# Optimization experiments

Measured on AMD Instinct MI355X. Metric: run time of the kernel, lower is better.

## Reference

```python
import jax, jax.numpy as jnp
import numpy as np

N_NODES = 100000
N_EDGES = 1_600_000
IN_C, HID_C, CLS_C = 128, 256, 64


def setup_inputs() -> dict:
    key = jax.random.key(0)
    ks = jax.random.split(key, 8)
    x = jax.random.normal(ks[0], (N_NODES, IN_C), dtype=jnp.float32)
    edge_index = jax.random.randint(ks[1], (2, N_EDGES), 0, N_NODES, dtype=jnp.int64)
    s1 = 1.0 / np.sqrt(IN_C)
    s2 = 1.0 / np.sqrt(HID_C)
    W1l = jax.random.uniform(ks[2], (IN_C, HID_C), jnp.float32, -s1, s1)
    W1r = jax.random.uniform(ks[3], (IN_C, HID_C), jnp.float32, -s1, s1)
    b1 = jnp.zeros((HID_C,), jnp.float32)
    W2l = jax.random.uniform(ks[4], (HID_C, CLS_C), jnp.float32, -s2, s2)
    W2r = jax.random.uniform(ks[5], (HID_C, CLS_C), jnp.float32, -s2, s2)
    b2 = jnp.zeros((CLS_C,), jnp.float32)
    return {"x": x, "edge_index": edge_index,
            "W1l": W1l, "W1r": W1r, "b1": b1,
            "W2l": W2l, "W2r": W2r, "b2": b2}


def _sage_conv(x, src, dst, Wl, Wr, b, num_nodes):
    # mean aggregation of source features onto destination nodes
    agg = jax.ops.segment_sum(x[src], dst, num_segments=num_nodes)  # [N, F]
    deg = jax.ops.segment_sum(jnp.ones((src.shape[0], 1), x.dtype), dst,
                              num_segments=num_nodes)               # [N, 1]
    agg = agg / jnp.maximum(deg, 1.0)  # zero-degree nodes -> 0
    return agg @ Wl + x @ Wr + b


def reference(x, edge_index, W1l, W1r, b1, W2l, W2r, b2):
    src, dst = edge_index[0], edge_index[1]
    n = x.shape[0]
    h = jax.nn.relu(_sage_conv(x, src, dst, W1l, W1r, b1, n))
    # dropout(p=0.5) is identity in eval mode
    out = _sage_conv(h, src, dst, W2l, W2r, b2, n)
    return jax.nn.sigmoid(out)
```

## Files before the change

### kernel.cpp

```cpp
#include <hip/hip_runtime.h>

typedef __attribute__((ext_vector_type(8))) short short8;
typedef __attribute__((ext_vector_type(4))) float floatx4;
typedef __attribute__((ext_vector_type(2))) float floatx2;

static __device__ __forceinline__ unsigned short f2bf(float f) {
  unsigned int u = __builtin_bit_cast(unsigned int, f);
  u += 0x7FFFu + ((u >> 16) & 1u);
  return (unsigned short)(u >> 16);
}
static __device__ __forceinline__ float bf2f(unsigned short s) {
  unsigned int u = ((unsigned int)s) << 16;
  return __builtin_bit_cast(float, u);
}
static __device__ __forceinline__ unsigned int pk4_fp8(float a, float b, float c, float d) {
  int lo = __builtin_amdgcn_cvt_pk_fp8_f32(a, b, 0, false);
  int hi = __builtin_amdgcn_cvt_pk_fp8_f32(c, d, 0, false);
  return (unsigned int)((lo & 0xffff) | ((hi & 0xffff) << 16));
}
static __device__ __forceinline__ floatx4 unpk4_fp8(unsigned int p) {
  floatx2 lo = __builtin_amdgcn_cvt_pk_f32_fp8((int)p, false);
  floatx2 hi = __builtin_amdgcn_cvt_pk_f32_fp8((int)p, true);
  floatx4 r = {lo.x, lo.y, hi.x, hi.y};
  return r;
}

#define NBUCK 2048
#define BIN_CHUNK 8192
#define SCAP 1536

__global__ __launch_bounds__(256) void binscatter(const int* __restrict__ src,
                                                  const int* __restrict__ dst,
                                                  int* __restrict__ bcnt,
                                                  unsigned int* __restrict__ staging,
                                                  int E) {
  __shared__ int h[NBUCK];
  __shared__ int cur[NBUCK];
  for (int i = threadIdx.x; i < NBUCK; i += 256) h[i] = 0;
  __syncthreads();
  int base = blockIdx.x * BIN_CHUNK;
  int end = base + BIN_CHUNK; if (end > E) end = E;
  for (int i = base + threadIdx.x; i < end; i += 256)
    atomicAdd(&h[dst[i] >> 6], 1);
  __syncthreads();
  for (int i = threadIdx.x; i < NBUCK; i += 256)
    cur[i] = h[i] ? atomicAdd(&bcnt[i], h[i]) : 0;
  __syncthreads();
  for (int i = base + threadIdx.x; i < end; i += 256) {
    int d = dst[i], s = src[i];
    int b = d >> 6;
    int pos = atomicAdd(&cur[b], 1);
    if (pos < SCAP)
      staging[(size_t)b * SCAP + pos] = ((unsigned int)(d & 63) << 17) | (unsigned int)s;
  }
}

__global__ void convw(const float* __restrict__ W1l, const float* __restrict__ W1r,
                      const float* __restrict__ W2l, const float* __restrict__ W2r,
                      unsigned short* __restrict__ W1p, unsigned short* __restrict__ W2p) {
  int i = blockIdx.x * blockDim.x + threadIdx.x;
  if (i < 8192) {
    int lane = i & 63, ni = (i >> 6) & 1, kk = (i >> 7) & 7, w = i >> 10;
    int fm = lane & 15, fq = lane >> 4;
    int n = w * 32 + ni * 16 + fm;
    int k0 = kk * 32 + fq * 8;
    unsigned short r[8];
#pragma unroll
    for (int j = 0; j < 8; j++) {
      int k = k0 + j;
      float v = (k < 128) ? W1l[k * 256 + n] : W1r[(k - 128) * 256 + n];
      r[j] = f2bf(v);
    }
    *reinterpret_cast<uint4*>(W1p + (size_t)i * 8) = *reinterpret_cast<uint4*>(r);
  } else if (i < 8192 + 4096) {
    int j2 = i - 8192;
    int lane = j2 & 63, kk = (j2 >> 6) & 7, w = j2 >> 9;
    int fm = lane & 15, fq = lane >> 4;
    int n = w * 16 + fm;
    int k0 = kk * 32 + fq * 8;
    unsigned short r[8];
#pragma unroll
    for (int j = 0; j < 8; j++) {
      int k = k0 + j;
      float v = (n < 64) ? W2l[k * 64 + n] : W2r[k * 64 + (n - 64)];
      r[j] = f2bf(v);
    }
    *reinterpret_cast<uint4*>(W2p + (size_t)j2 * 8) = *reinterpret_cast<uint4*>(r);
  }
}

__global__ void convx(const float* __restrict__ x, unsigned int* __restrict__ xq,
                      unsigned short* __restrict__ xbf, int n_nodes) {
  int i = blockIdx.x * blockDim.x + threadIdx.x;
  if (i < n_nodes * 32) {
    int node = i >> 5, c4 = (i & 31) * 4;
    float4 v = *reinterpret_cast<const float4*>(x + (size_t)node * 128 + c4);
    xq[i] = pk4_fp8(v.x, v.y, v.z, v.w);
    unsigned short r[4] = { f2bf(v.x), f2bf(v.y), f2bf(v.z), f2bf(v.w) };
    *reinterpret_cast<uint2*>(xbf + (size_t)node * 128 + c4) =
        *reinterpret_cast<uint2*>(r);
  }
}

#define LDSW 264
__global__ __launch_bounds__(512, 6) void gemm_fused(const unsigned short* __restrict__ xbf,
                                                     const uint4* __restrict__ xq,
                                                     const unsigned int* __restrict__ staging,
                                                     const int* __restrict__ bcnt,
                                                     const unsigned short* __restrict__ W1p,
                                                     const unsigned short* __restrict__ W2p,
                                                     const float* __restrict__ b1,
                                                     unsigned char* __restrict__ zq,
                                                     unsigned short* __restrict__ rb,
                                                     int M) {
  __shared__ unsigned short smem[64 * LDSW];
  __shared__ int eidx[SCAP];
  __shared__ int h64[64], rstart[64], cur64[64];
  const int tid = threadIdx.x;
  const int lane = tid & 63;
  const int wave = tid >> 6;
  const int m0 = blockIdx.x * 64;
  const int fm = lane & 15;
  const int fq = lane >> 4;
  const int base = blockIdx.x * SCAP;
  int cnt = bcnt[blockIdx.x]; if (cnt > SCAP) cnt = SCAP;
  const short8* __restrict__ W1v = reinterpret_cast<const short8*>(W1p);
  const short8* __restrict__ W2v = reinterpret_cast<const short8*>(W2p);

  if (tid < 64) h64[tid] = 0;
  __syncthreads();

  unsigned int ew0 = 0, ew1 = 0, ew2 = 0;
  const int i0 = tid, i1 = tid + 512, i2 = tid + 1024;
  if (i0 < cnt) ew0 = staging[base + i0];
  if (i1 < cnt) ew1 = staging[base + i1];
  if (i2 < cnt) ew2 = staging[base + i2];

#pragma unroll
  for (int j = 0; j < 2; j++) {
    int c = j * 512 + tid;
    int row = c >> 4, u4 = c & 15;
    int gr = m0 + row; if (gr >= M) gr = M - 1;
    uint4 v = *reinterpret_cast<const uint4*>(xbf + (size_t)gr * 128 + u4 * 8);
    *reinterpret_cast<uint4*>(&smem[row * LDSW + 128 + u4 * 8]) = v;
  }

  if (i0 < cnt) atomicAdd(&h64[ew0 >> 17], 1);
  if (i1 < cnt) atomicAdd(&h64[ew1 >> 17], 1);
  if (i2 < cnt) atomicAdd(&h64[ew2 >> 17], 1);
  __syncthreads();

  if (tid < 64) {
    int v = h64[tid];
    int s = v;
#pragma unroll
    for (int off = 1; off < 64; off <<= 1) {
      int o = __shfl_up(s, off, 64);
      if (tid >= off) s += o;
    }
    int excl = s - v;
    rstart[tid] = excl;
    cur64[tid] = excl;
  }
  __syncthreads();

  if (i0 < cnt) { int p = atomicAdd(&cur64[ew0 >> 17], 1); eidx[p] = (int)(ew0 & 0x1FFFFu); }
  if (i1 < cnt) { int p = atomicAdd(&cur64[ew1 >> 17], 1); eidx[p] = (int)(ew1 & 0x1FFFFu); }
  if (i2 < cnt) { int p = atomicAdd(&cur64[ew2 >> 17], 1); eidx[p] = (int)(ew2 & 0x1FFFFu); }
  __syncthreads();

  {
    const int grp = lane >> 3;
    const int ch4 = lane & 7;
    int row = wave * 8 + grp;
    int e0l = rstart[row];
    int e1l = e0l + h64[row];
    floatx4 a0[4] = {{0,0,0,0},{0,0,0,0},{0,0,0,0},{0,0,0,0}};
    floatx4 a1[4] = {{0,0,0,0},{0,0,0,0},{0,0,0,0},{0,0,0,0}};
    for (int e = e0l; e < e1l; e += 8) {
      uint4 pb[8];
#pragma unroll
      for (int j = 0; j < 8; j++) {
        int t = e + j; if (t >= e1l) t = e1l - 1;
        int s = eidx[t];
        pb[j] = xq[(s << 3) | ch4];
      }
      int rem = e1l - e;
#pragma unroll
      for (int j = 0; j < 8; j++) {
        if (j < rem) {
          floatx4* acc = (j & 1) ? a1 : a0;
          acc[0] += unpk4_fp8(pb[j].x);
          acc[1] += unpk4_fp8(pb[j].y);
          acc[2] += unpk4_fp8(pb[j].z);
          acc[3] += unpk4_fp8(pb[j].w);
        }
      }
    }
    int d = e1l - e0l; if (d < 1) d = 1;
    float sc = 1.0f / (float)d;
    unsigned short r[16];
#pragma unroll
    for (int j = 0; j < 4; j++) {
      floatx4 a = a0[j] + a1[j];
      r[4 * j + 0] = f2bf(a.x * sc); r[4 * j + 1] = f2bf(a.y * sc);
      r[4 * j + 2] = f2bf(a.z * sc); r[4 * j + 3] = f2bf(a.w * sc);
    }
    unsigned short* dstp = &smem[row * LDSW + ch4 * 16];
    *reinterpret_cast<uint4*>(dstp) = *reinterpret_cast<uint4*>(r);
    *reinterpret_cast<uint4*>(dstp + 8) = *reinterpret_cast<uint4*>(r + 8);
  }

  float bb[2];
#pragma unroll
  for (int ni = 0; ni < 2; ni++) bb[ni] = b1[wave * 32 + ni * 16 + fm];

  __syncthreads();

  floatx4 acc1[4][2] = {};
#pragma unroll 2
  for (int kk = 0; kk < 8; kk++) {
    short8 af[4], bfr[2];
#pragma unroll
    for (int mi = 0; mi < 4; mi++)
      af[mi] = *reinterpret_cast<const short8*>(
          &smem[(mi * 16 + fm) * LDSW + kk * 32 + fq * 8]);
#pragma unroll
    for (int ni = 0; ni < 2; ni++)
      bfr[ni] = W1v[((wave * 8 + kk) * 2 + ni) * 64 + lane];
#pragma unroll
    for (int mi = 0; mi < 4; mi++)
#pragma unroll
      for (int ni = 0; ni < 2; ni++)
        acc1[mi][ni] = __builtin_amdgcn_mfma_f32_16x16x32_bf16(af[mi], bfr[ni],
                                                               acc1[mi][ni], 0, 0, 0);
  }

  __syncthreads();

#pragma unroll
  for (int mi = 0; mi < 4; mi++)
#pragma unroll
    for (int ni = 0; ni < 2; ni++)
#pragma unroll
      for (int r = 0; r < 4; r++) {
        float v = acc1[mi][ni][r] + bb[ni];
        v = v > 0.f ? v : 0.f;
        smem[(mi * 16 + fq * 4 + r) * LDSW + wave * 32 + ni * 16 + fm] = f2bf(v);
      }
  __syncthreads();

  floatx4 acc2[4] = {};
#pragma unroll 2
  for (int kk = 0; kk < 8; kk++) {
    short8 hf[4];
#pragma unroll
    for (int mi = 0; mi < 4; mi++)
      hf[mi] = *reinterpret_cast<const short8*>(
          &smem[(mi * 16 + fm) * LDSW + kk * 32 + fq * 8]);
    short8 wf = W2v[(wave * 8 + kk) * 64 + lane];
#pragma unroll
    for (int mi = 0; mi < 4; mi++)
      acc2[mi] = __builtin_amdgcn_mfma_f32_16x16x32_bf16(hf[mi], wf, acc2[mi], 0, 0, 0);
  }

#pragma unroll
  for (int mi = 0; mi < 4; mi++)
#pragma unroll
    for (int r = 0; r < 4; r++) {
      int grow = m0 + mi * 16 + fq * 4 + r;
      if (grow < M) {
        float v = acc2[mi][r];
        if (wave < 4) {
          int col = wave * 16 + fm;
          int b8 = __builtin_amdgcn_cvt_pk_fp8_f32(v, v, 0, false);
          zq[grow * 64 + col] = (unsigned char)(b8 & 0xff);
        } else {
          int col = (wave - 4) * 16 + fm;
          rb[grow * 64 + col] = f2bf(v);
        }
      }
    }
}

__global__ __launch_bounds__(512, 6) void agg2_final(const uint2* __restrict__ zq2,
                                                     const unsigned short* __restrict__ rb,
                                                     const unsigned int* __restrict__ staging,
                                                     const int* __restrict__ bcnt,
                                                     const float* __restrict__ b2,
                                                     float* __restrict__ out, int n_nodes) {
  __shared__ int eidx[SCAP];
  __shared__ int h64[64], rstart[64], cur64[64];
  const int tid = threadIdx.x;
  const int lane = tid & 63;
  const int wave = tid >> 6;
  const int m0 = blockIdx.x * 64;
  const int base = blockIdx.x * SCAP;
  int cnt = bcnt[blockIdx.x]; if (cnt > SCAP) cnt = SCAP;

  if (tid < 64) h64[tid] = 0;
  __syncthreads();

  unsigned int ew0 = 0, ew1 = 0, ew2 = 0;
  const int i0 = tid, i1 = tid + 512, i2 = tid + 1024;
  if (i0 < cnt) ew0 = staging[base + i0];
  if (i1 < cnt) ew1 = staging[base + i1];
  if (i2 < cnt) ew2 = staging[base + i2];
  if (i0 < cnt) atomicAdd(&h64[ew0 >> 17], 1);
  if (i1 < cnt) atomicAdd(&h64[ew1 >> 17], 1);
  if (i2 < cnt) atomicAdd(&h64[ew2 >> 17], 1);
  __syncthreads();

  if (tid < 64) {
    int v = h64[tid];
    int s = v;
#pragma unroll
    for (int off = 1; off < 64; off <<= 1) {
      int o = __shfl_up(s, off, 64);
      if (tid >= off) s += o;
    }
    rstart[tid] = s - v;
    cur64[tid] = s - v;
  }
  __syncthreads();

  if (i0 < cnt) { int p = atomicAdd(&cur64[ew0 >> 17], 1); eidx[p] = (int)(ew0 & 0x1FFFFu); }
  if (i1 < cnt) { int p = atomicAdd(&cur64[ew1 >> 17], 1); eidx[p] = (int)(ew1 & 0x1FFFFu); }
  if (i2 < cnt) { int p = atomicAdd(&cur64[ew2 >> 17], 1); eidx[p] = (int)(ew2 & 0x1FFFFu); }
  __syncthreads();

  const int grp = lane >> 3;
  const int ch = lane & 7;
  int row = wave * 8 + grp;
  int w = m0 + row;
  if (w >= n_nodes) return;
  int e0l = rstart[row];
  int e1l = e0l + h64[row];
  floatx4 a0[2] = {{0,0,0,0},{0,0,0,0}};
  floatx4 a1[2] = {{0,0,0,0},{0,0,0,0}};
  for (int e = e0l; e < e1l; e += 8) {
    uint2 pb[8];
#pragma unroll
    for (int j = 0; j < 8; j++) {
      int t = e + j; if (t >= e1l) t = e1l - 1;
      int s = eidx[t];
      pb[j] = zq2[(s << 3) | ch];
    }
    int rem = e1l - e;
#pragma unroll
    for (int j = 0; j < 8; j++) {
      if (j < rem) {
        floatx4* acc = (j & 1) ? a1 : a0;
        acc[0] += unpk4_fp8(pb[j].x);
        acc[1] += unpk4_fp8(pb[j].y);
      }
    }
  }
  int d = e1l - e0l; if (d < 1) d = 1;
  float sc = 1.0f / (float)d;
  int c0 = ch * 8;
  uint4 rr = *reinterpret_cast<const uint4*>(rb + (size_t)w * 64 + c0);
  float4 bvA = *reinterpret_cast<const float4*>(b2 + c0);
  float4 bvB = *reinterpret_cast<const float4*>(b2 + c0 + 4);
  floatx4 s0 = a0[0] + a1[0];
  floatx4 s1 = a0[1] + a1[1];
  float4 oA, oB;
  oA.x = 1.0f / (1.0f + __expf(-(s0.x * sc + bf2f((unsigned short)(rr.x & 0xffff)) + bvA.x)));
  oA.y = 1.0f / (1.0f + __expf(-(s0.y * sc + bf2f((unsigned short)(rr.x >> 16)) + bvA.y)));
  oA.z = 1.0f / (1.0f + __expf(-(s0.z * sc + bf2f((unsigned short)(rr.y & 0xffff)) + bvA.z)));
  oA.w = 1.0f / (1.0f + __expf(-(s0.w * sc + bf2f((unsigned short)(rr.y >> 16)) + bvA.w)));
  oB.x = 1.0f / (1.0f + __expf(-(s1.x * sc + bf2f((unsigned short)(rr.z & 0xffff)) + bvB.x)));
  oB.y = 1.0f / (1.0f + __expf(-(s1.y * sc + bf2f((unsigned short)(rr.z >> 16)) + bvB.y)));
  oB.z = 1.0f / (1.0f + __expf(-(s1.z * sc + bf2f((unsigned short)(rr.w & 0xffff)) + bvB.z)));
  oB.w = 1.0f / (1.0f + __expf(-(s1.w * sc + bf2f((unsigned short)(rr.w >> 16)) + bvB.w)));
  float* op = out + (size_t)w * 64 + c0;
  *reinterpret_cast<float4*>(op) = oA;
  *reinterpret_cast<float4*>(op + 4) = oB;
}

extern "C" void kernel_launch(void* const* d_in, const int* in_sizes, int n_in,
                              void* d_out, int out_size, void* d_ws, size_t ws_size,
                              hipStream_t stream) {
  const float* x   = (const float*)d_in[0];
  const int*   ei  = (const int*)d_in[1];
  const float* W1l = (const float*)d_in[2];
  const float* W1r = (const float*)d_in[3];
  const float* b1  = (const float*)d_in[4];
  const float* W2l = (const float*)d_in[5];
  const float* W2r = (const float*)d_in[6];
  const float* b2  = (const float*)d_in[7];
  float* out = (float*)d_out;

  const int N = in_sizes[0] / 128;
  const int E = in_sizes[1] / 2;
  const int* src = ei;
  const int* dst = ei + E;

  char* wsb = (char*)d_ws;
  size_t off = 0;
  auto alloc = [&](size_t bytes) -> void* {
    void* p = wsb + off;
    off += (bytes + 511) & ~(size_t)511;
    return p;
  };
  int* bcnt     = (int*)alloc(NBUCK * 4);
  unsigned int* staging = (unsigned int*)alloc((size_t)NBUCK * SCAP * 4);
  unsigned short* W1p = (unsigned short*)alloc(256 * 256 * 2);
  unsigned short* W2p = (unsigned short*)alloc(128 * 256 * 2);
  unsigned int* xq    = (unsigned int*)alloc((size_t)N * 128);
  unsigned short* xbf = (unsigned short*)alloc((size_t)N * 128 * 2);
  unsigned char* zq   = (unsigned char*)alloc((size_t)N * 64);
  unsigned short* rb  = (unsigned short*)alloc((size_t)N * 64 * 2);
  (void)ws_size; (void)n_in; (void)out_size;

  const int ntiles = (N + 63) / 64;
  const int nchunks = (E + BIN_CHUNK - 1) / BIN_CHUNK;

  hipMemsetAsync(bcnt, 0, NBUCK * 4, stream);
  binscatter<<<nchunks, 256, 0, stream>>>(src, dst, bcnt, staging, E);

  convw<<<(8192 + 4096 + 255) / 256, 256, 0, stream>>>(W1l, W1r, W2l, W2r, W1p, W2p);
  convx<<<(N * 32 + 255) / 256, 256, 0, stream>>>(x, xq, xbf, N);

  gemm_fused<<<ntiles, 512, 0, stream>>>(xbf, (const uint4*)xq, staging, bcnt,
                                         W1p, W2p, b1, zq, rb, N);

  agg2_final<<<ntiles, 512, 0, stream>>>((const uint2*)zq, rb, staging, bcnt,
                                         b2, out, N);
}
```

Before: 229.0 us.

## Locally sort edges by bucket in LDS before scattering; fuse conversion kernels

The binning kernel now counts edges per bucket, prefix-scans the counts in shared memory, places each edge into a bucket-sorted shared buffer, and then writes contiguous runs to the global staging area, so global stores are coalesced instead of scattered. The chunk size is halved so the extra shared-memory buffers fit and more blocks are launched. The x and weight conversion kernels are merged into one launch to remove one kernel launch. The cost is extra LDS traffic, several more barriers in the scan, and lower occupancy per block because of the larger shared-memory footprint.

```diff
diff --git a/kernel.cpp b/kernel.cpp
--- a/kernel.cpp
+++ b/kernel.cpp
@@ -26,7 +26,7 @@
 }
 
 #define NBUCK 2048
-#define BIN_CHUNK 8192
+#define BIN_CHUNK 4096
 #define SCAP 1536
 
 __global__ __launch_bounds__(256) void binscatter(const int* __restrict__ src,
@@ -35,30 +35,73 @@
                                                   unsigned int* __restrict__ staging,
                                                   int E) {
   __shared__ int h[NBUCK];
-  __shared__ int cur[NBUCK];
-  for (int i = threadIdx.x; i < NBUCK; i += 256) h[i] = 0;
-  __syncthreads();
-  int base = blockIdx.x * BIN_CHUNK;
+  __shared__ int lstart[NBUCK];
+  __shared__ int lcur[NBUCK];
+  __shared__ int gbase[NBUCK];
+  __shared__ int ps[256];
+  __shared__ unsigned int sorted[BIN_CHUNK];
+  __shared__ unsigned short bkt[BIN_CHUNK];
+  const int t = threadIdx.x;
+  for (int i = t; i < NBUCK; i += 256) h[i] = 0;
+  __syncthreads();
+  const int base = blockIdx.x * BIN_CHUNK;
   int end = base + BIN_CHUNK; if (end > E) end = E;
-  for (int i = base + threadIdx.x; i < end; i += 256)
+  const int n = end - base;
+  for (int i = base + t; i < end; i += 256)
     atomicAdd(&h[dst[i] >> 6], 1);
   __syncthreads();
-  for (int i = threadIdx.x; i < NBUCK; i += 256)
-    cur[i] = h[i] ? atomicAdd(&bcnt[i], h[i]) : 0;
-  __syncthreads();
-  for (int i = base + threadIdx.x; i < end; i += 256) {
+  int v[8]; int tsum = 0;
+#pragma unroll
+  for (int j = 0; j < 8; j++) { v[j] = h[t * 8 + j]; tsum += v[j]; }
+  ps[t] = tsum;
+  __syncthreads();
+  for (int off = 1; off < 256; off <<= 1) {
+    int xx = (t >= off) ? ps[t - off] : 0;
+    __syncthreads();
+    ps[t] += xx;
+    __syncthreads();
+  }
+  int run = ps[t] - tsum;
+#pragma unroll
+  for (int j = 0; j < 8; j++) {
+    lstart[t * 8 + j] = run; lcur[t * 8 + j] = run; run += v[j];
+  }
+  __syncthreads();
+  for (int i = t; i < NBUCK; i += 256)
+    gbase[i] = h[i] ? atomicAdd(&bcnt[i], h[i]) : 0;
+  for (int i = base + t; i < end; i += 256) {
     int d = dst[i], s = src[i];
     int b = d >> 6;
-    int pos = atomicAdd(&cur[b], 1);
-    if (pos < SCAP)
-      staging[(size_t)b * SCAP + pos] = ((unsigned int)(d & 63) << 17) | (unsigned int)s;
-  }
-}
-
-__global__ void convw(const float* __restrict__ W1l, const float* __restrict__ W1r,
-                      const float* __restrict__ W2l, const float* __restrict__ W2r,
-                      unsigned short* __restrict__ W1p, unsigned short* __restrict__ W2p) {
-  int i = blockIdx.x * blockDim.x + threadIdx.x;
+    int p = atomicAdd(&lcur[b], 1);
+    sorted[p] = ((unsigned int)(d & 63) << 17) | (unsigned int)s;
+    bkt[p] = (unsigned short)b;
+  }
+  __syncthreads();
+  for (int p = t; p < n; p += 256) {
+    int b = bkt[p];
+    int g = gbase[b] + (p - lstart[b]);
+    if (g < SCAP) staging[(size_t)b * SCAP + g] = sorted[p];
+  }
+}
+
+__global__ void convxw(const float* __restrict__ x, unsigned int* __restrict__ xq,
+                       unsigned short* __restrict__ xbf,
+                       const float* __restrict__ W1l, const float* __restrict__ W1r,
+                       const float* __restrict__ W2l, const float* __restrict__ W2r,
+                       unsigned short* __restrict__ W1p, unsigned short* __restrict__ W2p,
+                       int n_nodes) {
+  int gi = blockIdx.x * blockDim.x + threadIdx.x;
+  const int xwork = n_nodes * 32;
+  if (gi < xwork) {
+    int node = gi >> 5, c4 = (gi & 31) * 4;
+    float4 v = *reinterpret_cast<const float4*>(x + (size_t)node * 128 + c4);
+    xq[gi] = pk4_fp8(v.x, v.y, v.z, v.w);
+    unsigned short r[4] = { f2bf(v.x), f2bf(v.y), f2bf(v.z), f2bf(v.w) };
+    *reinterpret_cast<uint2*>(xbf + (size_t)node * 128 + c4) =
+        *reinterpret_cast<uint2*>(r);
+    return;
+  }
+  int i = gi - xwork;
   if (i < 8192) {
     int lane = i & 63, ni = (i >> 6) & 1, kk = (i >> 7) & 7, w = i >> 10;
     int fm = lane & 15, fq = lane >> 4;
@@ -86,19 +129,6 @@
       r[j] = f2bf(v);
     }
     *reinterpret_cast<uint4*>(W2p + (size_t)j2 * 8) = *reinterpret_cast<uint4*>(r);
-  }
-}
-
-__global__ void convx(const float* __restrict__ x, unsigned int* __restrict__ xq,
-                      unsigned short* __restrict__ xbf, int n_nodes) {
-  int i = blockIdx.x * blockDim.x + threadIdx.x;
-  if (i < n_nodes * 32) {
-    int node = i >> 5, c4 = (i & 31) * 4;
-    float4 v = *reinterpret_cast<const float4*>(x + (size_t)node * 128 + c4);
-    xq[i] = pk4_fp8(v.x, v.y, v.z, v.w);
-    unsigned short r[4] = { f2bf(v.x), f2bf(v.y), f2bf(v.z), f2bf(v.w) };
-    *reinterpret_cast<uint2*>(xbf + (size_t)node * 128 + c4) =
-        *reinterpret_cast<uint2*>(r);
   }
 }
 
@@ -415,12 +445,12 @@
 
   const int ntiles = (N + 63) / 64;
   const int nchunks = (E + BIN_CHUNK - 1) / BIN_CHUNK;
+  const int convblocks = (N * 32 + 8192 + 4096 + 255) / 256;
 
   hipMemsetAsync(bcnt, 0, NBUCK * 4, stream);
   binscatter<<<nchunks, 256, 0, stream>>>(src, dst, bcnt, staging, E);
 
-  convw<<<(8192 + 4096 + 255) / 256, 256, 0, stream>>>(W1l, W1r, W2l, W2r, W1p, W2p);
-  convx<<<(N * 32 + 255) / 256, 256, 0, stream>>>(x, xq, xbf, N);
+  convxw<<<convblocks, 256, 0, stream>>>(x, xq, xbf, W1l, W1r, W2l, W2r, W1p, W2p, N);
 
   gemm_fused<<<ntiles, 512, 0, stream>>>(xbf, (const uint4*)xq, staging, bcnt,
                                          W1p, W2p, b1, zq, rb, N);
```

New measurement: 217.1 us. -5.2%, faster.
